# Kernel tuning notes

Hardware: AMD Instinct MI355X
Metric: run time of the kernel (lower is better)

## Reference

```python
import jax, jax.numpy as jnp
import numpy as np


def _hann(n_fft):
    # torch.hann_window default is periodic: 0.5*(1 - cos(2*pi*n/N))
    n = jnp.arange(n_fft, dtype=jnp.float32)
    return 0.5 * (1.0 - jnp.cos(2.0 * jnp.pi * n / n_fft))


def setup_inputs() -> dict:
    key = jax.random.key(0)
    k1, k2 = jax.random.split(key)
    B, T = 2, 131072
    hop = 256
    n_bins = 257  # n_fft // 2 + 1 with n_fft = 512
    ex = jax.random.normal(k1, (B, T), dtype=jnp.float32)
    log_mag = jax.random.normal(k2, (B, T // hop, n_bins), dtype=jnp.float32) * 0.5
    return {"ex": ex, "log_mag": log_mag, "hop_length": hop}


def reference(ex, log_mag, hop_length):
    # ex: [B, T], log_mag: [B, F, n_fft//2+1]
    B, T = ex.shape
    # zero-phase FIR: irfft of magnitude, then center with fftshift
    mag = jnp.exp(log_mag)
    fir = jnp.fft.irfft(mag, axis=-1)            # [B, F, n_fft]
    n_fft = fir.shape[-1]
    fir = jnp.fft.fftshift(fir, axes=-1)
    kernel = fir * _hann(n_fft)                  # [B, F, n_fft]

    padding = (n_fft - 1) // 2
    padded = jnp.pad(ex, ((0, 0), (padding, padding)))
    win_len = n_fft + hop_length - 1
    n_frames = (padded.shape[1] - win_len) // hop_length + 1
    kernel = kernel[:, :n_frames]                # [B, Fr, n_fft]

    # gather sliding windows: out[b,f,j] = sum_k padded[b, f*hop + j + k] * kernel[b,f,k]
    idx = (jnp.arange(n_frames) * hop_length)[:, None, None] \
        + jnp.arange(hop_length)[None, :, None] \
        + jnp.arange(n_fft)[None, None, :]       # [Fr, hop, n_fft]
    windows = padded[:, idx]                     # [B, Fr, hop, n_fft]
    out = jnp.einsum('bfjk,bfk->bfj', windows, kernel)
    return out.reshape(B, n_frames * hop_length)
```

## Files before the change

kernel.cpp:

```cpp
#include <hip/hip_runtime.h>

#define NFFT    512
#define NBINS   257
#define HOP     256
#define NFRAMES 511
#define TSAMP   131072

__device__ __forceinline__ int SWZ(int i) { return i + ((i >> 5) << 2); }

__global__ __launch_bounds__(256)
void ltv_fir(const float* __restrict__ ex,
             const float* __restrict__ log_mag,
             float* __restrict__ out)
{
    __shared__ float s_d[2][132];
    __shared__ float s_c[2];
    __shared__ float s_ker[512];
    __shared__ float s_ex[864];
    __shared__ float s_part[16][260];

    const int tid = threadIdx.x;
    const int bf  = blockIdx.x;
    const int b   = bf / NFRAMES;
    const int f   = bf - b * NFRAMES;

    const float* lm  = log_mag + ((size_t)b * 512 + f) * NBINS;
    const float* exb = ex + (size_t)b * TSAMP;

    if (tid < 192) {
        const int gw = f * HOP - 256 + tid * 4;
        float4 q = make_float4(0.f, 0.f, 0.f, 0.f);
        if (gw >= 0) q = *(const float4*)&exb[gw];
        const int wb = tid * 4 - 1;
        if (tid > 0) s_ex[SWZ(wb)] = q.x;
        s_ex[SWZ(wb + 1)] = q.y;
        s_ex[SWZ(wb + 2)] = q.z;
        s_ex[SWZ(wb + 3)] = q.w;
    } else {
        #pragma unroll
        for (int it = 0; it < 3; ++it) {
            const int s2 = (tid - 192) + 64 * it;
            if (s2 < 134) {
                if (s2 == 132)      s_c[0] = __expf(lm[0]);
                else if (s2 == 133) s_c[1] = __expf(lm[256]);
                else if (s2 == 0 || s2 >= 129) { s_d[0][s2] = 0.f; s_d[1][s2] = 0.f; }
                else if (s2 == 128) { const float v = __expf(lm[128]); s_d[0][128] = v; s_d[1][128] = v; }
                else {
                    const float a  = __expf(lm[s2]);
                    const float c0 = __expf(lm[256 - s2]);
                    const float sg = (s2 & 1) ? -1.f : 1.f;
                    s_d[0][s2] = sg * (a + c0);
                    s_d[1][s2] = sg * (a - c0);
                }
            }
        }
    }
    __syncthreads();

    if (tid <= 128) {
        const int wid  = tid >> 6;
        const int lane = tid & 63;
        const int n    = (wid == 2) ? 128 : 2 * lane + wid;
        const float t  = __cosf(3.14159265358979323846f * (float)n * (1.0f / 256.0f));
        const float k2 = 2.0f * t;
        const float* dsel = s_d[n & 1];
        float ce = 1.0f, co = t, E = 0.0f, O = 0.0f;
        #pragma unroll 3
        for (int m = 0; m < 132; m += 4) {
            float4 dd = *(const float4*)&dsel[m];
            E = fmaf(dd.x, ce, E);
            O = fmaf(dd.y, co, O);
            float ce2 = fmaf(k2, co,  -ce);
            float co2 = fmaf(k2, ce2, -co);
            E = fmaf(dd.z, ce2, E);
            O = fmaf(dd.w, co2, O);
            ce = fmaf(k2, co2, -ce2);
            co = fmaf(k2, ce,  -co2);
        }
        const float p    = (n & 1) ? -1.f : 1.f;
        const float cst  = s_c[0] + p * s_c[1];
        const float v_lo = (cst + 2.f * (E + O)) * (0.5f * (1.f - t)) * (1.f / 512.f);
        const float v_hi = (cst + 2.f * (E - O)) * (0.5f * (1.f + t)) * (1.f / 512.f);
        s_ker[n]       = v_lo;
        s_ker[256 - n] = v_hi;
        if (n > 0) { s_ker[256 + n] = v_hi; s_ker[512 - n] = v_lo; }
    }
    __syncthreads();

    {
        const int g   = tid >> 4;
        const int lt  = tid & 15;
        const int kb  = g * 32;
        const int off = kb + lt * 16;
        float w[20];
        #pragma unroll
        for (int c = 0; c < 5; ++c)
            *(float4*)&w[4 * c] = *(const float4*)&s_ex[SWZ(off + 4 * c)];
        float acc[16];
        #pragma unroll
        for (int r = 0; r < 16; ++r) acc[r] = 0.0f;
        #pragma unroll
        for (int kc = 0; kc < 32; kc += 4) {
            const float4 kq = *(const float4*)&s_ker[kb + kc];
            #pragma unroll
            for (int r = 0; r < 16; ++r)
                acc[r] = fmaf(w[r], kq.x, fmaf(w[r + 1], kq.y,
                         fmaf(w[r + 2], kq.z, fmaf(w[r + 3], kq.w, acc[r]))));
            if (kc < 28) {
                #pragma unroll
                for (int i = 0; i < 16; ++i) w[i] = w[i + 4];
                *(float4*)&w[16] = *(const float4*)&s_ex[SWZ(off + kc + 20)];
            }
        }
        #pragma unroll
        for (int c = 0; c < 4; ++c)
            *(float4*)&s_part[g][lt * 16 + 4 * c] =
                make_float4(acc[4 * c], acc[4 * c + 1], acc[4 * c + 2], acc[4 * c + 3]);
    }
    __syncthreads();

    float r = 0.0f;
    #pragma unroll
    for (int gg = 0; gg < 16; ++gg) r += s_part[gg][tid];
    out[((size_t)b * NFRAMES + f) * HOP + tid] = r;
}

extern "C" void kernel_launch(void* const* d_in, const int* in_sizes, int n_in,
                              void* d_out, int out_size, void* d_ws, size_t ws_size,
                              hipStream_t stream)
{
    const float* ex      = (const float*)d_in[0];
    const float* log_mag = (const float*)d_in[1];
    float* out = (float*)d_out;

    dim3 grid(2 * NFRAMES);
    dim3 block(256);
    hipLaunchKernelGGL(ltv_fir, grid, block, 0, stream, ex, log_mag, out);
}
```

Before: 12.86 us.

## Split FIR kernel generation and convolution into two kernels with half-frame blocks

Moves per-frame kernel synthesis into its own launch, which writes the 512-tap windowed filters to workspace. A second kernel then runs the convolution with two blocks per frame, each computing 128 outputs with 128 threads, which doubles the block count and shrinks per-block shared memory. The aim is to remove the serial synthesis-then-convolve dependency inside one block and improve occupancy, at the cost of an extra launch and a global-memory round trip for the filters. The 129th cosine term is now handled by a separate thread-127 path.

Result: slower. 15.74 us (+22.4%).

```diff
diff --git a/kernel.cpp b/kernel.cpp
--- a/kernel.cpp
+++ b/kernel.cpp
@@ -8,59 +8,41 @@
 
 __device__ __forceinline__ int SWZ(int i) { return i + ((i >> 5) << 2); }
 
-__global__ __launch_bounds__(256)
-void ltv_fir(const float* __restrict__ ex,
-             const float* __restrict__ log_mag,
-             float* __restrict__ out)
+__global__ __launch_bounds__(128)
+void genker(const float* __restrict__ log_mag, float* __restrict__ wsK)
 {
     __shared__ float s_d[2][132];
     __shared__ float s_c[2];
-    __shared__ float s_ker[512];
-    __shared__ float s_ex[864];
-    __shared__ float s_part[16][260];
 
     const int tid = threadIdx.x;
     const int bf  = blockIdx.x;
     const int b   = bf / NFRAMES;
     const int f   = bf - b * NFRAMES;
+    const float* lm = log_mag + ((size_t)b * 512 + f) * NBINS;
 
-    const float* lm  = log_mag + ((size_t)b * 512 + f) * NBINS;
-    const float* exb = ex + (size_t)b * TSAMP;
-
-    if (tid < 192) {
-        const int gw = f * HOP - 256 + tid * 4;
-        float4 q = make_float4(0.f, 0.f, 0.f, 0.f);
-        if (gw >= 0) q = *(const float4*)&exb[gw];
-        const int wb = tid * 4 - 1;
-        if (tid > 0) s_ex[SWZ(wb)] = q.x;
-        s_ex[SWZ(wb + 1)] = q.y;
-        s_ex[SWZ(wb + 2)] = q.z;
-        s_ex[SWZ(wb + 3)] = q.w;
-    } else {
-        #pragma unroll
-        for (int it = 0; it < 3; ++it) {
-            const int s2 = (tid - 192) + 64 * it;
-            if (s2 < 134) {
-                if (s2 == 132)      s_c[0] = __expf(lm[0]);
-                else if (s2 == 133) s_c[1] = __expf(lm[256]);
-                else if (s2 == 0 || s2 >= 129) { s_d[0][s2] = 0.f; s_d[1][s2] = 0.f; }
-                else if (s2 == 128) { const float v = __expf(lm[128]); s_d[0][128] = v; s_d[1][128] = v; }
-                else {
-                    const float a  = __expf(lm[s2]);
-                    const float c0 = __expf(lm[256 - s2]);
-                    const float sg = (s2 & 1) ? -1.f : 1.f;
-                    s_d[0][s2] = sg * (a + c0);
-                    s_d[1][s2] = sg * (a - c0);
-                }
-            }
+    {
+        const int s2 = tid;
+        if (s2 == 0) { s_d[0][0] = 0.f; s_d[1][0] = 0.f; }
+        else {
+            const float a  = __expf(lm[s2]);
+            const float c0 = __expf(lm[256 - s2]);
+            const float sg = (s2 & 1) ? -1.f : 1.f;
+            s_d[0][s2] = sg * (a + c0);
+            s_d[1][s2] = sg * (a - c0);
+        }
+        if (tid < 6) {
+            const int s3 = 128 + tid;
+            if (s3 == 128) { const float v = __expf(lm[128]); s_d[0][128] = v; s_d[1][128] = v; }
+            else if (s3 < 132) { s_d[0][s3] = 0.f; s_d[1][s3] = 0.f; }
+            else if (s3 == 132) s_c[0] = __expf(lm[0]);
+            else                s_c[1] = __expf(lm[256]);
         }
     }
     __syncthreads();
 
-    if (tid <= 128) {
-        const int wid  = tid >> 6;
-        const int lane = tid & 63;
-        const int n    = (wid == 2) ? 128 : 2 * lane + wid;
+    float* wk = wsK + (size_t)bf * NFFT;
+    {
+        const int n    = tid;
         const float t  = __cosf(3.14159265358979323846f * (float)n * (1.0f / 256.0f));
         const float k2 = 2.0f * t;
         const float* dsel = s_d[n & 1];
@@ -81,17 +63,59 @@
         const float cst  = s_c[0] + p * s_c[1];
         const float v_lo = (cst + 2.f * (E + O)) * (0.5f * (1.f - t)) * (1.f / 512.f);
         const float v_hi = (cst + 2.f * (E - O)) * (0.5f * (1.f + t)) * (1.f / 512.f);
-        s_ker[n]       = v_lo;
-        s_ker[256 - n] = v_hi;
-        if (n > 0) { s_ker[256 + n] = v_hi; s_ker[512 - n] = v_lo; }
+        wk[n]       = v_lo;
+        wk[256 - n] = v_hi;
+        if (n > 0) { wk[256 + n] = v_hi; wk[512 - n] = v_lo; }
+    }
+    if (tid == 127) {
+        float E = 0.0f;
+        #pragma unroll 3
+        for (int m = 0; m < 132; m += 4) E += s_d[0][m] - s_d[0][m + 2];
+        const float v = (s_c[0] + s_c[1] + 2.f * E) * 0.5f * (1.f / 512.f);
+        wk[128] = v; wk[384] = v;
+    }
+}
+
+__global__ __launch_bounds__(128)
+void conv(const float* __restrict__ ex, const float* __restrict__ wsK,
+          float* __restrict__ out)
+{
+    __shared__ float s_ex[720];
+    __shared__ float s_K[576];
+    __shared__ float s_part[16][132];
+
+    const int tid = threadIdx.x;
+    const int hb  = blockIdx.x;
+    const int bf  = hb >> 1;
+    const int b   = bf / NFRAMES;
+    const int f   = bf - b * NFRAMES;
+    const int j0  = (hb & 1) << 7;
+
+    const float* exb = ex + (size_t)b * TSAMP;
+    const float* wk  = wsK + (size_t)bf * NFFT;
+
+    const int gbase = f * HOP + j0 - 256;
+    #pragma unroll
+    for (int t = tid; t < 160; t += 128) {
+        const int gw = gbase + 4 * t;
+        float4 q = make_float4(0.f, 0.f, 0.f, 0.f);
+        if (gw >= 0) q = *(const float4*)&exb[gw];
+        if (t > 0) s_ex[SWZ(4 * t - 1)] = q.x;
+        s_ex[SWZ(4 * t)]     = q.y;
+        s_ex[SWZ(4 * t + 1)] = q.z;
+        s_ex[SWZ(4 * t + 2)] = q.w;
+    }
+    {
+        float4 kq = *(const float4*)&wk[4 * tid];
+        *(float4*)&s_K[SWZ(4 * tid)] = kq;
     }
     __syncthreads();
 
     {
-        const int g   = tid >> 4;
-        const int lt  = tid & 15;
-        const int kb  = g * 32;
-        const int off = kb + lt * 16;
+        const int ot  = tid & 7;
+        const int kt  = tid >> 3;
+        const int kb  = kt * 32;
+        const int off = ot * 16 + kb;
         float w[20];
         #pragma unroll
         for (int c = 0; c < 5; ++c)
@@ -101,7 +125,7 @@
         for (int r = 0; r < 16; ++r) acc[r] = 0.0f;
         #pragma unroll
         for (int kc = 0; kc < 32; kc += 4) {
-            const float4 kq = *(const float4*)&s_ker[kb + kc];
+            const float4 kq = *(const float4*)&s_K[SWZ(kb + kc)];
             #pragma unroll
             for (int r = 0; r < 16; ++r)
                 acc[r] = fmaf(w[r], kq.x, fmaf(w[r + 1], kq.y,
@@ -114,15 +138,15 @@
         }
         #pragma unroll
         for (int c = 0; c < 4; ++c)
-            *(float4*)&s_part[g][lt * 16 + 4 * c] =
+            *(float4*)&s_part[kt][ot * 16 + 4 * c] =
                 make_float4(acc[4 * c], acc[4 * c + 1], acc[4 * c + 2], acc[4 * c + 3]);
     }
     __syncthreads();
 
     float r = 0.0f;
     #pragma unroll
-    for (int gg = 0; gg < 16; ++gg) r += s_part[gg][tid];
-    out[((size_t)b * NFRAMES + f) * HOP + tid] = r;
+    for (int p = 0; p < 16; ++p) r += s_part[p][tid];
+    out[((size_t)b * NFRAMES + f) * HOP + j0 + tid] = r;
 }
 
 extern "C" void kernel_launch(void* const* d_in, const int* in_sizes, int n_in,
@@ -131,9 +155,9 @@
 {
     const float* ex      = (const float*)d_in[0];
     const float* log_mag = (const float*)d_in[1];
-    float* out = (float*)d_out;
+    float* outp = (float*)d_out;
+    float* wsK  = (float*)d_ws;
 
-    dim3 grid(2 * NFRAMES);
-    dim3 block(256);
-    hipLaunchKernelGGL(ltv_fir, grid, block, 0, stream, ex, log_mag, out);
+    hipLaunchKernelGGL(genker, dim3(2 * NFRAMES), dim3(128), 0, stream, log_mag, wsK);
+    hipLaunchKernelGGL(conv,   dim3(4 * NFRAMES), dim3(128), 0, stream, ex, wsK, outp);
 }
```

## Process two frames per block with 128 threads each and larger register tiles

Applied to the files above, without the earlier changes.

Each 256-thread block now handles two frames, one per half, which halves the grid size. Each half uses 128 threads and each thread accumulates 32 outputs instead of 16, so every loaded window value is reused more in registers. All 128 threads of a half now share the exp/IRFFT setup, with one extra thread patching the n=128 kernel tap. The cost is more registers per thread and double the shared memory per block, which may lower occupancy; the grid also shrinks to 511 blocks.

New measurement: 13.60 us. +5.7%, slower.

```diff
diff --git a/kernel.cpp b/kernel.cpp
--- a/kernel.cpp
+++ b/kernel.cpp
@@ -9,61 +9,66 @@
 __device__ __forceinline__ int SWZ(int i) { return i + ((i >> 5) << 2); }
 
 __global__ __launch_bounds__(256)
-void ltv_fir(const float* __restrict__ ex,
-             const float* __restrict__ log_mag,
-             float* __restrict__ out)
+void ltv_fir2(const float* __restrict__ ex,
+              const float* __restrict__ log_mag,
+              float* __restrict__ out)
 {
-    __shared__ float s_d[2][132];
-    __shared__ float s_c[2];
-    __shared__ float s_ker[512];
-    __shared__ float s_ex[864];
-    __shared__ float s_part[16][260];
+    __shared__ float s_d[2][2][132];
+    __shared__ float s_c[2][2];
+    __shared__ float s_ker[2][512];
+    __shared__ float s_ex[2][872];
+    __shared__ float s_part[2][16][276];
 
-    const int tid = threadIdx.x;
-    const int bf  = blockIdx.x;
-    const int b   = bf / NFRAMES;
-    const int f   = bf - b * NFRAMES;
+    const int tid  = threadIdx.x;
+    const int half = tid >> 7;
+    const int ht   = tid & 127;
+    const int bf   = blockIdx.x * 2 + half;
+    const int b    = bf / NFRAMES;
+    const int f    = bf - b * NFRAMES;
 
     const float* lm  = log_mag + ((size_t)b * 512 + f) * NBINS;
     const float* exb = ex + (size_t)b * TSAMP;
 
-    if (tid < 192) {
-        const int gw = f * HOP - 256 + tid * 4;
-        float4 q = make_float4(0.f, 0.f, 0.f, 0.f);
-        if (gw >= 0) q = *(const float4*)&exb[gw];
-        const int wb = tid * 4 - 1;
-        if (tid > 0) s_ex[SWZ(wb)] = q.x;
-        s_ex[SWZ(wb + 1)] = q.y;
-        s_ex[SWZ(wb + 2)] = q.z;
-        s_ex[SWZ(wb + 3)] = q.w;
-    } else {
+    {
+        const int gbase = f * HOP - 256;
         #pragma unroll
-        for (int it = 0; it < 3; ++it) {
-            const int s2 = (tid - 192) + 64 * it;
-            if (s2 < 134) {
-                if (s2 == 132)      s_c[0] = __expf(lm[0]);
-                else if (s2 == 133) s_c[1] = __expf(lm[256]);
-                else if (s2 == 0 || s2 >= 129) { s_d[0][s2] = 0.f; s_d[1][s2] = 0.f; }
-                else if (s2 == 128) { const float v = __expf(lm[128]); s_d[0][128] = v; s_d[1][128] = v; }
-                else {
-                    const float a  = __expf(lm[s2]);
-                    const float c0 = __expf(lm[256 - s2]);
-                    const float sg = (s2 & 1) ? -1.f : 1.f;
-                    s_d[0][s2] = sg * (a + c0);
-                    s_d[1][s2] = sg * (a - c0);
-                }
+        for (int it = 0; it < 2; ++it) {
+            const int t = ht + 128 * it;
+            if (t < 193) {
+                const int gw = gbase + 4 * t;
+                float4 q = make_float4(0.f, 0.f, 0.f, 0.f);
+                if (gw >= 0 && gw + 3 < TSAMP) q = *(const float4*)&exb[gw];
+                if (t > 0) s_ex[half][SWZ(4 * t - 1)] = q.x;
+                s_ex[half][SWZ(4 * t)]     = q.y;
+                s_ex[half][SWZ(4 * t + 1)] = q.z;
+                s_ex[half][SWZ(4 * t + 2)] = q.w;
             }
+        }
+    }
+    {
+        if (ht == 0) { s_d[half][0][0] = 0.f; s_d[half][1][0] = 0.f; }
+        else {
+            const float a  = __expf(lm[ht]);
+            const float c0 = __expf(lm[256 - ht]);
+            const float sg = (ht & 1) ? -1.f : 1.f;
+            s_d[half][0][ht] = sg * (a + c0);
+            s_d[half][1][ht] = sg * (a - c0);
+        }
+        if (ht < 6) {
+            const int s3 = 128 + ht;
+            if (s3 == 128) { const float v = __expf(lm[128]); s_d[half][0][128] = v; s_d[half][1][128] = v; }
+            else if (s3 < 132) { s_d[half][0][s3] = 0.f; s_d[half][1][s3] = 0.f; }
+            else if (s3 == 132) s_c[half][0] = __expf(lm[0]);
+            else                s_c[half][1] = __expf(lm[256]);
         }
     }
     __syncthreads();
 
-    if (tid <= 128) {
-        const int wid  = tid >> 6;
-        const int lane = tid & 63;
-        const int n    = (wid == 2) ? 128 : 2 * lane + wid;
+    {
+        const int n    = 2 * (ht & 63) + (ht >> 6);
         const float t  = __cosf(3.14159265358979323846f * (float)n * (1.0f / 256.0f));
         const float k2 = 2.0f * t;
-        const float* dsel = s_d[n & 1];
+        const float* dsel = s_d[half][n & 1];
         float ce = 1.0f, co = t, E = 0.0f, O = 0.0f;
         #pragma unroll 3
         for (int m = 0; m < 132; m += 4) {
@@ -78,51 +83,65 @@
             co = fmaf(k2, ce,  -co2);
         }
         const float p    = (n & 1) ? -1.f : 1.f;
-        const float cst  = s_c[0] + p * s_c[1];
+        const float cst  = s_c[half][0] + p * s_c[half][1];
         const float v_lo = (cst + 2.f * (E + O)) * (0.5f * (1.f - t)) * (1.f / 512.f);
         const float v_hi = (cst + 2.f * (E - O)) * (0.5f * (1.f + t)) * (1.f / 512.f);
-        s_ker[n]       = v_lo;
-        s_ker[256 - n] = v_hi;
-        if (n > 0) { s_ker[256 + n] = v_hi; s_ker[512 - n] = v_lo; }
+        s_ker[half][n]       = v_lo;
+        s_ker[half][256 - n] = v_hi;
+        if (n > 0) { s_ker[half][256 + n] = v_hi; s_ker[half][512 - n] = v_lo; }
+        if (ht == 127) {
+            float E2 = 0.0f;
+            #pragma unroll 3
+            for (int m = 0; m < 132; m += 4) E2 += s_d[half][0][m] - s_d[half][0][m + 2];
+            const float v = (s_c[half][0] + s_c[half][1] + 2.f * E2) * 0.5f * (1.f / 512.f);
+            s_ker[half][128] = v; s_ker[half][384] = v;
+        }
     }
     __syncthreads();
 
     {
-        const int g   = tid >> 4;
-        const int lt  = tid & 15;
-        const int kb  = g * 32;
-        const int off = kb + lt * 16;
-        float w[20];
+        const int ot  = ht & 7;
+        const int kt  = ht >> 3;
+        const int kb  = kt * 32;
+        const int off = ot * 32 + kb;
+        float w[36];
         #pragma unroll
-        for (int c = 0; c < 5; ++c)
-            *(float4*)&w[4 * c] = *(const float4*)&s_ex[SWZ(off + 4 * c)];
-        float acc[16];
+        for (int c = 0; c < 9; ++c)
+            *(float4*)&w[4 * c] = *(const float4*)&s_ex[half][SWZ(off + 4 * c)];
+        float acc[32];
         #pragma unroll
-        for (int r = 0; r < 16; ++r) acc[r] = 0.0f;
+        for (int r = 0; r < 32; ++r) acc[r] = 0.0f;
         #pragma unroll
         for (int kc = 0; kc < 32; kc += 4) {
-            const float4 kq = *(const float4*)&s_ker[kb + kc];
+            const float4 kq = *(const float4*)&s_ker[half][kb + kc];
             #pragma unroll
-            for (int r = 0; r < 16; ++r)
+            for (int r = 0; r < 32; ++r)
                 acc[r] = fmaf(w[r], kq.x, fmaf(w[r + 1], kq.y,
                          fmaf(w[r + 2], kq.z, fmaf(w[r + 3], kq.w, acc[r]))));
             if (kc < 28) {
                 #pragma unroll
-                for (int i = 0; i < 16; ++i) w[i] = w[i + 4];
-                *(float4*)&w[16] = *(const float4*)&s_ex[SWZ(off + kc + 20)];
+                for (int i = 0; i < 32; ++i) w[i] = w[i + 4];
+                *(float4*)&w[32] = *(const float4*)&s_ex[half][SWZ(off + kc + 36)];
             }
         }
         #pragma unroll
-        for (int c = 0; c < 4; ++c)
-            *(float4*)&s_part[g][lt * 16 + 4 * c] =
+        for (int c = 0; c < 8; ++c)
+            *(float4*)&s_part[half][kt][ot * 32 + 4 * c] =
                 make_float4(acc[4 * c], acc[4 * c + 1], acc[4 * c + 2], acc[4 * c + 3]);
     }
     __syncthreads();
 
-    float r = 0.0f;
-    #pragma unroll
-    for (int gg = 0; gg < 16; ++gg) r += s_part[gg][tid];
-    out[((size_t)b * NFRAMES + f) * HOP + tid] = r;
+    {
+        float r0 = 0.0f, r1 = 0.0f;
+        #pragma unroll
+        for (int p = 0; p < 16; ++p) {
+            r0 += s_part[half][p][ht];
+            r1 += s_part[half][p][ht + 128];
+        }
+        float* ob = out + ((size_t)b * NFRAMES + f) * HOP;
+        ob[ht]       = r0;
+        ob[ht + 128] = r1;
+    }
 }
 
 extern "C" void kernel_launch(void* const* d_in, const int* in_sizes, int n_in,
@@ -131,9 +150,9 @@
 {
     const float* ex      = (const float*)d_in[0];
     const float* log_mag = (const float*)d_in[1];
-    float* out = (float*)d_out;
+    float* outp = (float*)d_out;
 
-    dim3 grid(2 * NFRAMES);
+    dim3 grid(NFRAMES);
     dim3 block(256);
-    hipLaunchKernelGGL(ltv_fir, grid, block, 0, stream, ex, log_mag, out);
+    hipLaunchKernelGGL(ltv_fir2, grid, block, 0, stream, ex, log_mag, outp);
 }
```
